# Kernel optimization log

Hardware: AMD Instinct MI355X
Metric: run time of the kernel (lower is better)

The kernel has to match this reference:

```python
import jax, jax.numpy as jnp
import numpy as np

SIZE_DICT = 512
DIM_DICT = 256
TEMPERATURE = 0.5
EPS = 1e-10


def setup_inputs() -> dict:
    key = jax.random.key(0)
    k1, k2, k3 = jax.random.split(key, 3)
    bs, dim_z, W, H = 32, DIM_DICT, 32, 32
    z_from_encoder = jax.random.normal(k1, (bs, dim_z, W, H), dtype=jnp.float32)
    kappa_q = jnp.ones((1,), dtype=jnp.float32)
    codebook = jax.random.normal(k2, (SIZE_DICT, DIM_DICT), dtype=jnp.float32)
    gumbel_u = jax.random.uniform(k3, (bs * W * H, SIZE_DICT), dtype=jnp.float32)
    return {"z_from_encoder": z_from_encoder, "kappa_q": kappa_q,
            "codebook": codebook, "gumbel_u": gumbel_u, "flg_train": 1}


def reference(z_from_encoder, kappa_q, codebook, gumbel_u, flg_train):
    bs, dim_z, W, H = z_from_encoder.shape
    # [bs, dim_z, W, H] -> [bs*W*H, dim_z]
    z_flat = jnp.transpose(z_from_encoder, (0, 2, 3, 1)).reshape(-1, dim_z)
    kq = jnp.clip(kappa_q, 1e-5, 1e5)  # scalar-ish [1]
    # L2-normalize codebook rows
    cb = codebook / jnp.linalg.norm(codebook, axis=1, keepdims=True)
    # logit = -distance = kappa * <z, c>   [N, K]
    logit = kq * (z_flat @ cb.T)
    logit = logit - jnp.max(logit, axis=-1, keepdims=True)
    logit = jnp.clip(logit, -50.0, 50.0)
    probabilities = jax.nn.softmax(logit, axis=-1)
    log_probabilities = jax.nn.log_softmax(logit, axis=-1)
    # training path: gumbel-softmax relaxation
    g = -jnp.log(-jnp.log(gumbel_u + EPS) + EPS)
    encodings = jax.nn.softmax((logit + g) / TEMPERATURE, axis=-1)
    z_quantized = (encodings @ cb).reshape(bs, W, H, dim_z)
    avg_probs = jnp.mean(jax.lax.stop_gradient(probabilities), axis=0)
    z_to_decoder = jnp.transpose(z_quantized, (0, 3, 1, 2))
    kld_discrete = jnp.sum(probabilities * log_probabilities) / bs
    kld_continuous = jnp.mean(
        jnp.sum(z_from_encoder * (z_from_encoder - z_to_decoder) * kq[0],
                axis=(1, 2, 3)))
    loss = kld_discrete + kld_continuous
    avg_probs = jnp.clip(avg_probs, 1e-10, None)
    perplexity = jnp.exp(-jnp.sum(avg_probs * jnp.log(avg_probs + 1e-10)))
    return z_to_decoder, loss, perplexity
```

## Files before the change

### kernel.cpp

```cpp
#include <hip/hip_runtime.h>
#include <stdint.h>


typedef float v4f __attribute__((ext_vector_type(4)));
typedef short v8s __attribute__((ext_vector_type(8)));

#define ZA_STR 264
#define L2_STR 520

__device__ __forceinline__ uint16_t f2bf(float x) {
  uint32_t u = __float_as_uint(x);
  u = u + 0x7fffu + ((u >> 16) & 1u);
  return (uint16_t)(u >> 16);
}
__device__ __forceinline__ float bf2f(uint16_t h) {
  return __uint_as_float(((uint32_t)h) << 16);
}


__global__ __launch_bounds__(64) void vq_prep(const float* __restrict__ cb,
                                              char* __restrict__ ws) {
  const int blk = blockIdx.x, t = threadIdx.x;
  uint16_t* cbn2 = (uint16_t*)ws;
  uint16_t* cbt2 = (uint16_t*)(ws + 262144);
  float* shadow = (float*)(ws + 524288);
  float* scal   = (float*)(ws + 557056);
  if (blk < 512) {
    const int c = blk;
    float v[4]; float s = 0.f;
#pragma unroll
    for (int i = 0; i < 4; i++) { v[i] = cb[c * 256 + t + 64 * i]; s += v[i] * v[i]; }
#pragma unroll
    for (int mm = 1; mm < 64; mm <<= 1) s += __shfl_xor(s, mm, 64);
    const float sc = 1.0f / sqrtf(s);
    const int w = c >> 7, ct = (c >> 4) & 7, mcol = c & 15;
    const int cc = c >> 6, k2 = (c >> 5) & 1, qq = (c >> 3) & 3, j2 = c & 7;
#pragma unroll
    for (int i = 0; i < 4; i++) {
      const int d = t + 64 * i;
      const uint16_t h = f2bf(v[i] * sc);
      const int ks = d >> 5, q3 = (d >> 3) & 3, j = d & 7;
      cbn2[((ks * 8 + ct) * 4 + w) * 512 + (q3 * 16 + mcol) * 8 + j] = h;
      const int wd = d >> 6, nt = (d >> 4) & 3, md = d & 15;
      cbt2[(((cc * 2 + k2) * 4 + nt) * 4 + wd) * 512 + (qq * 16 + md) * 8 + j2] = h;
    }
  } else if (blk < 528) {
    const int j = blk - 512;
#pragma unroll
    for (int i = 0; i < 8; i++) shadow[j * 512 + t + 64 * i] = 0.f;
  } else {
    if (t < 3) scal[t] = 0.f;
  }
}

__global__ __launch_bounds__(256, 3) void vq_main(const float* __restrict__ z,
                                                  const float* __restrict__ kappa,
                                                  const float* __restrict__ gum,
                                                  char* __restrict__ ws,
                                                  float* __restrict__ out) {
  __shared__ char s_buf0[32 * ZA_STR * 2];
  __shared__ char s_buf1[256 * 33 * 4];
  __shared__ float s_pm[128], s_pS[128], s_pT[128];
  __shared__ float s_M[32], s_rS[32], s_kd[32], s_rSe[32], s_red[8];

  const int t = threadIdx.x;
  const int w = t >> 6, lane = t & 63, q = lane >> 4, m = lane & 15;
  const int bi = blockIdx.x, b = bi >> 5, wh0 = (bi & 31) << 5;
  const int R0 = bi << 5;

  const uint16_t* cbn2 = (const uint16_t*)ws;
  const uint16_t* cbt2 = (const uint16_t*)(ws + 262144);
  float* shadow = (float*)(ws + 524288);
  float* scal   = (float*)(ws + 557056);

  uint16_t* za  = (uint16_t*)s_buf0;
  uint16_t* l2s = (uint16_t*)s_buf1;

  const float kq = fminf(fmaxf(kappa[0], 1e-5f), 1e5f);

  {
    float zs = 0.f;
    const int whb = (t & 7) << 2, dT = t >> 3;
    const float* zb = z + ((size_t)b << 18) + wh0 + whb;
#pragma unroll
    for (int s = 0; s < 8; s++) {
      const int d = dT + (s << 5);
      const float4 v = *(const float4*)(zb + (d << 10));
      zs += v.x * v.x + v.y * v.y + v.z * v.z + v.w * v.w;
      za[(whb + 0) * ZA_STR + d] = f2bf(v.x);
      za[(whb + 1) * ZA_STR + d] = f2bf(v.y);
      za[(whb + 2) * ZA_STR + d] = f2bf(v.z);
      za[(whb + 3) * ZA_STR + d] = f2bf(v.w);
    }
#pragma unroll
    for (int mm = 1; mm < 64; mm <<= 1) zs += __shfl_xor(zs, mm, 64);
    if (lane == 0) s_red[w] = zs;
  }
  __syncthreads();
  if (t == 0) atomicAdd(&scal[1], s_red[0] + s_red[1] + s_red[2] + s_red[3]);

  v4f acc0[8], acc1[8];
#pragma unroll
  for (int i = 0; i < 8; i++) { acc0[i] = (v4f)0.f; acc1[i] = (v4f)0.f; }
  {
    const uint16_t* bp  = cbn2 + (w << 9) + (lane << 3);
    const uint16_t* a0p = za + m * ZA_STR;
    const uint16_t* a1p = za + (m + 16) * ZA_STR;
#pragma unroll
    for (int ks = 0; ks < 8; ks++) {
      const v8s a0 = *(const v8s*)(a0p + (ks << 5) + (q << 3));
      const v8s a1 = *(const v8s*)(a1p + (ks << 5) + (q << 3));
#pragma unroll
      for (int ct = 0; ct < 8; ct++) {
        const v8s bf = *(const v8s*)(bp + (((ks << 3) + ct) << 11));
        acc0[ct] = __builtin_amdgcn_mfma_f32_16x16x32_bf16(a0, bf, acc0[ct], 0, 0, 0);
        acc1[ct] = __builtin_amdgcn_mfma_f32_16x16x32_bf16(a1, bf, acc1[ct], 0, 0, 0);
      }
    }
  }

  {
    auto stats_half = [&](v4f (&acc)[8], int half) {
#pragma unroll
      for (int reg = 0; reg < 4; reg++) {
        float mx = -1e30f;
#pragma unroll
        for (int ct = 0; ct < 8; ct++) mx = fmaxf(mx, kq * acc[ct][reg]);
#pragma unroll
        for (int mm = 1; mm < 16; mm <<= 1) mx = fmaxf(mx, __shfl_xor(mx, mm, 64));
        float S = 0.f, T = 0.f;
#pragma unroll
        for (int ct = 0; ct < 8; ct++) {
          const float d = kq * acc[ct][reg] - mx;
          const float e = __expf(d);
          S += e; T += d * e;
        }
#pragma unroll
        for (int mm = 1; mm < 16; mm <<= 1) { S += __shfl_xor(S, mm, 64); T += __shfl_xor(T, mm, 64); }
        if (m == 0) {
          const int r = half * 16 + q * 4 + reg;
          s_pm[(w << 5) + r] = mx; s_pS[(w << 5) + r] = S; s_pT[(w << 5) + r] = T;
        }
      }
    };
    stats_half(acc0, 0);
    stats_half(acc1, 1);
  }
  __syncthreads();
  if (t < 32) {
    float M = s_pm[t];
    M = fmaxf(M, s_pm[32 + t]); M = fmaxf(M, s_pm[64 + t]); M = fmaxf(M, s_pm[96 + t]);
    float S = 0.f, T = 0.f;
#pragma unroll
    for (int ww = 0; ww < 4; ww++) {
      const float dm = s_pm[ww * 32 + t] - M;
      const float al = __expf(dm);
      S += s_pS[ww * 32 + t] * al;
      T += (s_pT[ww * 32 + t] + dm * s_pS[ww * 32 + t]) * al;
    }
    const float rS = 1.0f / S;
    s_M[t] = M; s_rS[t] = rS; s_kd[t] = T * rS - __logf(S);
  }
  __syncthreads();

  {
    const int c0 = w << 7;
    float colacc[8];
#pragma unroll
    for (int i = 0; i < 8; i++) colacc[i] = 0.f;
    auto pass2_half = [&](v4f (&acc)[8], int half) {
#pragma unroll
      for (int reg = 0; reg < 4; reg++) {
        const int r = half * 16 + q * 4 + reg;
        const float Mr = s_M[r], rSr = s_rS[r];
        uint16_t* lrow = l2s + r * L2_STR + c0 + m;
#pragma unroll
        for (int ct = 0; ct < 8; ct++) {
          const float d = fmaxf(kq * acc[ct][reg] - Mr, -50.0f);
          const float e = __expf(d);
          colacc[ct] += e * rSr;
          lrow[ct << 4] = f2bf(d);
        }
      }
    };
    pass2_half(acc0, 0);
    pass2_half(acc1, 1);
#pragma unroll
    for (int i = 0; i < 8; i++) {
      colacc[i] += __shfl_xor(colacc[i], 16, 64);
      colacc[i] += __shfl_xor(colacc[i], 32, 64);
    }
    if (q == 0) {
      float* sh = shadow + ((bi & 15) << 9) + c0 + m;
#pragma unroll
      for (int i = 0; i < 8; i++) atomicAdd(&sh[i << 4], colacc[i]);
    }
    if (w == 0) {
      float kd = s_kd[lane & 31];
#pragma unroll
      for (int mm = 1; mm < 64; mm <<= 1) kd += __shfl_xor(kd, mm, 64);
      if (lane == 0) atomicAdd(&scal[0], 0.5f * kd);
    }
  }
  __syncthreads();

  short* s_ec = (short*)s_buf0;
  const int rme = t >> 3, ce8 = (t & 7) << 3;
  const float* gr = gum + (size_t)(R0 + rme) * 512 + ce8;
  const float mxr = s_M[rme];
  float se = 0.f, ce = 0.f;
  v4f acc2a[4], acc2b[4];
#pragma unroll
  for (int i = 0; i < 4; i++) { acc2a[i] = (v4f)0.f; acc2b[i] = (v4f)0.f; }

  auto compute_chunk = [&](int cc) {
    const int buf = cc & 1;
    const float4 g0 = *(const float4*)(gr + (cc << 6));
    const float4 g1 = *(const float4*)(gr + (cc << 6) + 4);
    const float gg[8] = {g0.x, g0.y, g0.z, g0.w, g1.x, g1.y, g1.z, g1.w};
    union { v8s v; uint16_t u[8]; } lv, eb;
    lv.v = *(const v8s*)(l2s + rme * L2_STR + (cc << 6) + ce8);
#pragma unroll
    for (int i = 0; i < 8; i++) {
      const float l2 = bf2f(lv.u[i]);
      const float L = -__logf(gg[i] + 1e-10f) + 1e-10f;
      const float er = __expf(2.0f * (l2 - __logf(L)));
      se += er; ce += er * (l2 + mxr);
      eb.u[i] = f2bf(er);
    }
    *(v8s*)(s_ec + buf * 2304 + rme * 72 + ce8) = eb.v;
  };
  auto mfma_chunk = [&](int cc) {
    const int buf = cc & 1;
#pragma unroll
    for (int ks = 0; ks < 2; ks++) {
      const v8s a0 = *(const v8s*)(s_ec + buf * 2304 + m * 72 + (ks << 5) + (q << 3));
      const v8s a1 = *(const v8s*)(s_ec + buf * 2304 + (m + 16) * 72 + (ks << 5) + (q << 3));
      const uint16_t* bp2 = cbt2 + (((cc << 1) + ks) << 13) + (w << 9) + (lane << 3);
#pragma unroll
      for (int nt = 0; nt < 4; nt++) {
        const v8s bf = *(const v8s*)(bp2 + (nt << 11));
        acc2a[nt] = __builtin_amdgcn_mfma_f32_16x16x32_bf16(a0, bf, acc2a[nt], 0, 0, 0);
        acc2b[nt] = __builtin_amdgcn_mfma_f32_16x16x32_bf16(a1, bf, acc2b[nt], 0, 0, 0);
      }
    }
  };

  compute_chunk(0);
  __syncthreads();
#pragma unroll 1
  for (int cc = 0; cc < 8; cc++) {
    mfma_chunk(cc);
    if (cc < 7) compute_chunk(cc + 1);
    __syncthreads();
  }

#pragma unroll
  for (int mm = 1; mm < 8; mm <<= 1) { se += __shfl_xor(se, mm, 64); ce += __shfl_xor(ce, mm, 64); }
  {
    float cr = ((t & 7) == 0) ? (ce / se) : 0.f;
#pragma unroll
    for (int mm = 8; mm < 64; mm <<= 1) cr += __shfl_xor(cr, mm, 64);
    if (lane == 0) s_red[w] = cr;
    if ((t & 7) == 0) s_rSe[rme] = 1.0f / se;
  }
  __syncthreads();
  if (t == 0) atomicAdd(&scal[2], s_red[0] + s_red[1] + s_red[2] + s_red[3]);

  {
    float* zqT = (float*)s_buf1;
    const int d0 = w << 6;
    float rsA[4], rsB[4];
#pragma unroll
    for (int reg = 0; reg < 4; reg++) {
      rsA[reg] = s_rSe[q * 4 + reg];
      rsB[reg] = s_rSe[16 + q * 4 + reg];
    }
#pragma unroll
    for (int nt = 0; nt < 4; nt++) {
      const int d = d0 + (nt << 4) + m;
#pragma unroll
      for (int reg = 0; reg < 4; reg++) {
        zqT[d * 33 + q * 4 + reg]      = acc2a[nt][reg] * rsA[reg];
        zqT[d * 33 + 16 + q * 4 + reg] = acc2b[nt][reg] * rsB[reg];
      }
    }
  }
  __syncthreads();
  {
    const int whb = (t & 7) << 2, dT = t >> 3;
    float* ob = out + ((size_t)b << 18) + wh0 + whb;
    const float* zqT = (const float*)s_buf1;
#pragma unroll
    for (int s = 0; s < 8; s++) {
      const int d = dT + (s << 5);
      const float* zr = zqT + d * 33 + whb;
      float4 v; v.x = zr[0]; v.y = zr[1]; v.z = zr[2]; v.w = zr[3];
      *(float4*)(ob + (d << 10)) = v;
    }
  }
}

__global__ __launch_bounds__(512) void vq_final(const float* __restrict__ kappa,
                                                char* __restrict__ ws,
                                                float* __restrict__ out) {
  __shared__ float red[8];
  const int t = threadIdx.x;
  const float* shadow = (const float*)(ws + 524288);
  const float* scal   = (const float*)(ws + 557056);
  float s = 0.f;
#pragma unroll
  for (int j = 0; j < 16; j++) s += shadow[(j << 9) + t];
  float avg = fmaxf(s * (1.0f / 32768.0f), 1e-10f);
  float term = avg * __logf(avg + 1e-10f);
#pragma unroll
  for (int mm = 1; mm < 64; mm <<= 1) term += __shfl_xor(term, mm, 64);
  if ((t & 63) == 0) red[t >> 6] = term;
  __syncthreads();
  if (t == 0) {
    float H = 0.f;
#pragma unroll
    for (int i = 0; i < 8; i++) H += red[i];
    const float perpl = __expf(-H);
    const float kq = fminf(fmaxf(kappa[0], 1e-5f), 1e5f);
    const float loss = (scal[0] + kq * scal[1] - scal[2]) * (1.0f / 32.0f);
    out[8388608] = loss;
    out[8388609] = perpl;
  }
}

extern "C" void kernel_launch(void* const* d_in, const int* in_sizes, int n_in,
                              void* d_out, int out_size, void* d_ws, size_t ws_size,
                              hipStream_t stream) {
  const float* z     = (const float*)d_in[0];
  const float* kappa = (const float*)d_in[1];
  const float* cb    = (const float*)d_in[2];
  const float* gum   = (const float*)d_in[3];
  char* ws = (char*)d_ws;
  float* out = (float*)d_out;
  hipLaunchKernelGGL(vq_prep,  dim3(529),  dim3(64),  0, stream, cb, ws);
  hipLaunchKernelGGL(vq_main,  dim3(1024), dim3(256), 0, stream, z, kappa, gum, ws, out);
  hipLaunchKernelGGL(vq_final, dim3(1),    dim3(512), 0, stream, kappa, ws, out);
}
```

Baseline: 215.4 us.

## Shrink LDS footprint, prefetch gumbel noise, split codebook prep into vectorized pass

The codebook prep is split into a norm kernel and a second kernel that writes the bf16 swizzled layouts with packed 16-byte stores. The main kernel aliases its shared buffers so it can target four blocks per CU. Gumbel uniforms are prefetched into registers before the first GEMM. The second-phase loop now works on 16 chunks of 32 columns and is fully unrolled, and kappa is folded into the accumulators once. The LDS transpose for the output is removed in favour of direct strided global stores, which may coalesce worse. An extra kernel launch is added.

New measurement: 207.4 us. -3.7%, faster.

```diff
diff --git a/kernel.cpp b/kernel.cpp
--- a/kernel.cpp
+++ b/kernel.cpp
@@ -4,9 +4,11 @@
 
 typedef float v4f __attribute__((ext_vector_type(4)));
 typedef short v8s __attribute__((ext_vector_type(8)));
+typedef short v4s __attribute__((ext_vector_type(4)));
 
 #define ZA_STR 264
 #define L2_STR 520
+#define EC_STR 40
 
 __device__ __forceinline__ uint16_t f2bf(float x) {
   uint32_t u = __float_as_uint(x);
@@ -18,32 +20,19 @@
 }
 
 
-__global__ __launch_bounds__(64) void vq_prep(const float* __restrict__ cb,
-                                              char* __restrict__ ws) {
+__global__ __launch_bounds__(64) void vq_prep0(const float* __restrict__ cb,
+                                               char* __restrict__ ws) {
   const int blk = blockIdx.x, t = threadIdx.x;
-  uint16_t* cbn2 = (uint16_t*)ws;
-  uint16_t* cbt2 = (uint16_t*)(ws + 262144);
   float* shadow = (float*)(ws + 524288);
   float* scal   = (float*)(ws + 557056);
+  float* rnorm  = (float*)(ws + 557072);
   if (blk < 512) {
-    const int c = blk;
-    float v[4]; float s = 0.f;
-#pragma unroll
-    for (int i = 0; i < 4; i++) { v[i] = cb[c * 256 + t + 64 * i]; s += v[i] * v[i]; }
+    float s = 0.f;
+#pragma unroll
+    for (int i = 0; i < 4; i++) { const float v = cb[blk * 256 + t + 64 * i]; s += v * v; }
 #pragma unroll
     for (int mm = 1; mm < 64; mm <<= 1) s += __shfl_xor(s, mm, 64);
-    const float sc = 1.0f / sqrtf(s);
-    const int w = c >> 7, ct = (c >> 4) & 7, mcol = c & 15;
-    const int cc = c >> 6, k2 = (c >> 5) & 1, qq = (c >> 3) & 3, j2 = c & 7;
-#pragma unroll
-    for (int i = 0; i < 4; i++) {
-      const int d = t + 64 * i;
-      const uint16_t h = f2bf(v[i] * sc);
-      const int ks = d >> 5, q3 = (d >> 3) & 3, j = d & 7;
-      cbn2[((ks * 8 + ct) * 4 + w) * 512 + (q3 * 16 + mcol) * 8 + j] = h;
-      const int wd = d >> 6, nt = (d >> 4) & 3, md = d & 15;
-      cbt2[(((cc * 2 + k2) * 4 + nt) * 4 + wd) * 512 + (qq * 16 + md) * 8 + j2] = h;
-    }
+    if (t == 0) rnorm[blk] = 1.0f / sqrtf(s);
   } else if (blk < 528) {
     const int j = blk - 512;
 #pragma unroll
@@ -53,14 +42,47 @@
   }
 }
 
-__global__ __launch_bounds__(256, 3) void vq_main(const float* __restrict__ z,
+__global__ __launch_bounds__(256) void vq_prep1(const float* __restrict__ cb,
+                                                char* __restrict__ ws) {
+  const int b = blockIdx.x, t = threadIdx.x;
+  uint16_t* cbn2 = (uint16_t*)ws;
+  uint16_t* cbt2 = (uint16_t*)(ws + 262144);
+  const float* rnorm = (const float*)(ws + 557072);
+  union { v8s v; uint16_t u[8]; } pk;
+  if (b < 64) {
+    const int g = b * 256 + t;
+    const int code = g >> 5, dch = g & 31;
+    const float rn = rnorm[code];
+    const float4 f0 = *(const float4*)(cb + code * 256 + dch * 8);
+    const float4 f1 = *(const float4*)(cb + code * 256 + dch * 8 + 4);
+    pk.u[0] = f2bf(f0.x * rn); pk.u[1] = f2bf(f0.y * rn);
+    pk.u[2] = f2bf(f0.z * rn); pk.u[3] = f2bf(f0.w * rn);
+    pk.u[4] = f2bf(f1.x * rn); pk.u[5] = f2bf(f1.y * rn);
+    pk.u[6] = f2bf(f1.z * rn); pk.u[7] = f2bf(f1.w * rn);
+    const int w = code >> 7, ct = (code >> 4) & 7, mcol = code & 15;
+    const int ks = dch >> 2, q3 = dch & 3;
+    *(v8s*)(cbn2 + ((ks * 8 + ct) * 4 + w) * 512 + (q3 * 16 + mcol) * 8) = pk.v;
+  } else {
+    const int g = (b - 64) * 256 + t;
+    const int cgroup = g >> 8, d = g & 255;
+#pragma unroll
+    for (int j = 0; j < 8; j++) {
+      const int c = cgroup * 8 + j;
+      pk.u[j] = f2bf(cb[c * 256 + d] * rnorm[c]);
+    }
+    const int cc = cgroup >> 2, qq = cgroup & 3;
+    const int wd = d >> 6, nt = (d >> 4) & 3, md = d & 15;
+    *(v8s*)(cbt2 + ((cc * 4 + nt) * 4 + wd) * 512 + (qq * 16 + md) * 8) = pk.v;
+  }
+}
+
+__global__ __launch_bounds__(256, 4) void vq_main(const float* __restrict__ z,
                                                   const float* __restrict__ kappa,
                                                   const float* __restrict__ gum,
                                                   char* __restrict__ ws,
                                                   float* __restrict__ out) {
-  __shared__ char s_buf0[32 * ZA_STR * 2];
-  __shared__ char s_buf1[256 * 33 * 4];
-  __shared__ float s_pm[128], s_pS[128], s_pT[128];
+  __shared__ char s_A[33280];
+  __shared__ char s_B[5120];
   __shared__ float s_M[32], s_rS[32], s_kd[32], s_rSe[32], s_red[8];
 
   const int t = threadIdx.x;
@@ -73,10 +95,17 @@
   float* shadow = (float*)(ws + 524288);
   float* scal   = (float*)(ws + 557056);
 
-  uint16_t* za  = (uint16_t*)s_buf0;
-  uint16_t* l2s = (uint16_t*)s_buf1;
+  uint16_t* za  = (uint16_t*)s_A;
+  uint16_t* l2s = (uint16_t*)s_A;
+  float* s_pm = (float*)s_B;
+  float* s_pS = (float*)s_B + 128;
+  float* s_pT = (float*)s_B + 256;
+  short* s_ec = (short*)s_B;
 
   const float kq = fminf(fmaxf(kappa[0], 1e-5f), 1e5f);
+
+  const int row = t >> 3, c4 = (t & 7) << 2;
+  const float* gbase = gum + (size_t)(R0 + row) * 512 + c4;
 
   {
     float zs = 0.f;
@@ -96,6 +125,11 @@
     for (int mm = 1; mm < 64; mm <<= 1) zs += __shfl_xor(zs, mm, 64);
     if (lane == 0) s_red[w] = zs;
   }
+
+  float4 gq[4];
+#pragma unroll
+  for (int i = 0; i < 4; i++) gq[i] = *(const float4*)(gbase + (i << 5));
+
   __syncthreads();
   if (t == 0) atomicAdd(&scal[1], s_red[0] + s_red[1] + s_red[2] + s_red[3]);
 
@@ -118,6 +152,8 @@
       }
     }
   }
+#pragma unroll
+  for (int i = 0; i < 8; i++) { acc0[i] *= kq; acc1[i] *= kq; }
 
   {
     auto stats_half = [&](v4f (&acc)[8], int half) {
@@ -125,13 +161,13 @@
       for (int reg = 0; reg < 4; reg++) {
         float mx = -1e30f;
 #pragma unroll
-        for (int ct = 0; ct < 8; ct++) mx = fmaxf(mx, kq * acc[ct][reg]);
+        for (int ct = 0; ct < 8; ct++) mx = fmaxf(mx, acc[ct][reg]);
 #pragma unroll
         for (int mm = 1; mm < 16; mm <<= 1) mx = fmaxf(mx, __shfl_xor(mx, mm, 64));
         float S = 0.f, T = 0.f;
 #pragma unroll
         for (int ct = 0; ct < 8; ct++) {
-          const float d = kq * acc[ct][reg] - mx;
+          const float d = acc[ct][reg] - mx;
           const float e = __expf(d);
           S += e; T += d * e;
         }
@@ -176,7 +212,7 @@
         uint16_t* lrow = l2s + r * L2_STR + c0 + m;
 #pragma unroll
         for (int ct = 0; ct < 8; ct++) {
-          const float d = fmaxf(kq * acc[ct][reg] - Mr, -50.0f);
+          const float d = fmaxf(acc[ct][reg] - Mr, -50.0f);
           const float e = __expf(d);
           colacc[ct] += e * rSr;
           lrow[ct << 4] = f2bf(d);
@@ -204,10 +240,7 @@
   }
   __syncthreads();
 
-  short* s_ec = (short*)s_buf0;
-  const int rme = t >> 3, ce8 = (t & 7) << 3;
-  const float* gr = gum + (size_t)(R0 + rme) * 512 + ce8;
-  const float mxr = s_M[rme];
+  const float mxr = s_M[row];
   float se = 0.f, ce = 0.f;
   v4f acc2a[4], acc2b[4];
 #pragma unroll
@@ -215,43 +248,40 @@
 
   auto compute_chunk = [&](int cc) {
     const int buf = cc & 1;
-    const float4 g0 = *(const float4*)(gr + (cc << 6));
-    const float4 g1 = *(const float4*)(gr + (cc << 6) + 4);
-    const float gg[8] = {g0.x, g0.y, g0.z, g0.w, g1.x, g1.y, g1.z, g1.w};
-    union { v8s v; uint16_t u[8]; } lv, eb;
-    lv.v = *(const v8s*)(l2s + rme * L2_STR + (cc << 6) + ce8);
-#pragma unroll
-    for (int i = 0; i < 8; i++) {
-      const float l2 = bf2f(lv.u[i]);
-      const float L = -__logf(gg[i] + 1e-10f) + 1e-10f;
+    const float4 u = gq[cc & 3];
+    const float uu[4] = {u.x, u.y, u.z, u.w};
+    union { v4s v; uint16_t h[4]; } lv, eb;
+    lv.v = *(const v4s*)(l2s + row * L2_STR + (cc << 5) + c4);
+#pragma unroll
+    for (int i = 0; i < 4; i++) {
+      const float l2 = bf2f(lv.h[i]);
+      const float L = -__logf(uu[i] + 1e-10f) + 1e-10f;
       const float er = __expf(2.0f * (l2 - __logf(L)));
       se += er; ce += er * (l2 + mxr);
-      eb.u[i] = f2bf(er);
-    }
-    *(v8s*)(s_ec + buf * 2304 + rme * 72 + ce8) = eb.v;
+      eb.h[i] = f2bf(er);
+    }
+    *(v4s*)(s_ec + buf * 1280 + row * EC_STR + c4) = eb.v;
+    if (cc + 4 < 16) gq[cc & 3] = *(const float4*)(gbase + ((cc + 4) << 5));
   };
   auto mfma_chunk = [&](int cc) {
     const int buf = cc & 1;
-#pragma unroll
-    for (int ks = 0; ks < 2; ks++) {
-      const v8s a0 = *(const v8s*)(s_ec + buf * 2304 + m * 72 + (ks << 5) + (q << 3));
-      const v8s a1 = *(const v8s*)(s_ec + buf * 2304 + (m + 16) * 72 + (ks << 5) + (q << 3));
-      const uint16_t* bp2 = cbt2 + (((cc << 1) + ks) << 13) + (w << 9) + (lane << 3);
-#pragma unroll
-      for (int nt = 0; nt < 4; nt++) {
-        const v8s bf = *(const v8s*)(bp2 + (nt << 11));
-        acc2a[nt] = __builtin_amdgcn_mfma_f32_16x16x32_bf16(a0, bf, acc2a[nt], 0, 0, 0);
-        acc2b[nt] = __builtin_amdgcn_mfma_f32_16x16x32_bf16(a1, bf, acc2b[nt], 0, 0, 0);
-      }
+    const v8s a0 = *(const v8s*)(s_ec + buf * 1280 + m * EC_STR + (q << 3));
+    const v8s a1 = *(const v8s*)(s_ec + buf * 1280 + (m + 16) * EC_STR + (q << 3));
+    const uint16_t* bp2 = cbt2 + (cc << 13) + (w << 9) + (lane << 3);
+#pragma unroll
+    for (int nt = 0; nt < 4; nt++) {
+      const v8s bf = *(const v8s*)(bp2 + (nt << 11));
+      acc2a[nt] = __builtin_amdgcn_mfma_f32_16x16x32_bf16(a0, bf, acc2a[nt], 0, 0, 0);
+      acc2b[nt] = __builtin_amdgcn_mfma_f32_16x16x32_bf16(a1, bf, acc2b[nt], 0, 0, 0);
     }
   };
 
   compute_chunk(0);
   __syncthreads();
-#pragma unroll 1
-  for (int cc = 0; cc < 8; cc++) {
+#pragma unroll
+  for (int cc = 0; cc < 16; cc++) {
     mfma_chunk(cc);
-    if (cc < 7) compute_chunk(cc + 1);
+    if (cc < 15) compute_chunk(cc + 1);
     __syncthreads();
   }
 
@@ -262,13 +292,13 @@
 #pragma unroll
     for (int mm = 8; mm < 64; mm <<= 1) cr += __shfl_xor(cr, mm, 64);
     if (lane == 0) s_red[w] = cr;
-    if ((t & 7) == 0) s_rSe[rme] = 1.0f / se;
+    if ((t & 7) == 0) s_rSe[row] = 1.0f / se;
   }
   __syncthreads();
   if (t == 0) atomicAdd(&scal[2], s_red[0] + s_red[1] + s_red[2] + s_red[3]);
 
   {
-    float* zqT = (float*)s_buf1;
+    float* ob = out + ((size_t)b << 18) + wh0;
     const int d0 = w << 6;
     float rsA[4], rsB[4];
 #pragma unroll
@@ -281,22 +311,9 @@
       const int d = d0 + (nt << 4) + m;
 #pragma unroll
       for (int reg = 0; reg < 4; reg++) {
-        zqT[d * 33 + q * 4 + reg]      = acc2a[nt][reg] * rsA[reg];
-        zqT[d * 33 + 16 + q * 4 + reg] = acc2b[nt][reg] * rsB[reg];
+        ob[(d << 10) + q * 4 + reg]      = acc2a[nt][reg] * rsA[reg];
+        ob[(d << 10) + 16 + q * 4 + reg] = acc2b[nt][reg] * rsB[reg];
       }
-    }
-  }
-  __syncthreads();
-  {
-    const int whb = (t & 7) << 2, dT = t >> 3;
-    float* ob = out + ((size_t)b << 18) + wh0 + whb;
-    const float* zqT = (const float*)s_buf1;
-#pragma unroll
-    for (int s = 0; s < 8; s++) {
-      const int d = dT + (s << 5);
-      const float* zr = zqT + d * 33 + whb;
-      float4 v; v.x = zr[0]; v.y = zr[1]; v.z = zr[2]; v.w = zr[3];
-      *(float4*)(ob + (d << 10)) = v;
     }
   }
 }
@@ -338,7 +355,8 @@
   const float* gum   = (const float*)d_in[3];
   char* ws = (char*)d_ws;
   float* out = (float*)d_out;
-  hipLaunchKernelGGL(vq_prep,  dim3(529),  dim3(64),  0, stream, cb, ws);
+  hipLaunchKernelGGL(vq_prep0, dim3(529),  dim3(64),  0, stream, cb, ws);
+  hipLaunchKernelGGL(vq_prep1, dim3(128),  dim3(256), 0, stream, cb, ws);
   hipLaunchKernelGGL(vq_main,  dim3(1024), dim3(256), 0, stream, z, kappa, gum, ws, out);
   hipLaunchKernelGGL(vq_final, dim3(1),    dim3(512), 0, stream, kappa, ws, out);
 }
```
